# Kernel tuning notes

Measured on AMD Instinct MI355X. Metric: run time of the kernel, lower is better.

The kernel has to match this reference:

```python
import jax, jax.numpy as jnp
import numpy as np


def setup_inputs() -> dict:
    key = jax.random.key(0)
    d_model, state_dim, L = 512, 64, 2048
    scale = 1.0 / np.sqrt(state_dim)
    k1, k2, k3, k4, k5 = jax.random.split(key, 5)
    log_dt_min, log_dt_max = np.log(1e-3), np.log(0.1)
    return {
        "Lambda_re": jax.random.normal(k1, (d_model, state_dim), jnp.float32),
        "Lambda_im": jax.random.normal(k2, (d_model, state_dim), jnp.float32),
        "B_re": jax.random.normal(k3, (d_model, state_dim), jnp.float32) * scale,
        "B_im": jnp.zeros((d_model, state_dim), jnp.float32),
        "C_re": jax.random.normal(k4, (d_model, state_dim), jnp.float32) * scale,
        "C_im": jnp.zeros((d_model, state_dim), jnp.float32),
        "D": jnp.ones((d_model,), jnp.float32),
        "log_dt": jax.random.uniform(k5, (d_model,), jnp.float32, log_dt_min, log_dt_max),
        "L": L,
    }


def reference(Lambda_re, Lambda_im, B_re, B_im, C_re, C_im, D, log_dt, L):
    # Bilinear (Tustin) discretization of the diagonal SSM
    lam = (-jax.nn.softplus(Lambda_re) + 1j * Lambda_im).astype(jnp.complex64)  # (d, n)
    B = (B_re + 1j * B_im).astype(jnp.complex64)
    C = (C_re + 1j * C_im).astype(jnp.complex64)
    dt = jnp.exp(log_dt)[:, None]                 # (d, 1)
    half = 0.5 * dt * lam
    denom = 1.0 - half
    a_bar = (1.0 + half) / denom                  # (d, n)
    b_bar = dt / denom * B                        # (d, n)
    # Vandermonde power sum: K[d, l] = Re sum_n (C*b_bar)[d, n] * a_bar[d, n]**l
    k = jnp.arange(L, dtype=jnp.float32)
    a_pow = jnp.exp(jnp.log(a_bar)[:, :, None] * k)   # (d, n, L) complex
    K = jnp.einsum("dn,dnl->dl", C * b_bar, a_pow).real  # (d, L)
    return (K, D)
```

## Files before the change

kernel.cpp:

```cpp
#include <hip/hip_runtime.h>
#include <math.h>


#define STATE_DIM 64
#define BLOCK 256

__global__ __launch_bounds__(BLOCK) void lssl_kernel(
    const float* __restrict__ Lre, const float* __restrict__ Lim,
    const float* __restrict__ Bre, const float* __restrict__ Bim,
    const float* __restrict__ Cre, const float* __restrict__ Cim,
    const float* __restrict__ Dv,  const float* __restrict__ log_dt,
    float* __restrict__ out, int d_model, int L)
{
    const int d   = blockIdx.x;
    const int tid = threadIdx.x;

    __shared__ float s_log2r[STATE_DIM];
    __shared__ float s_threv[STATE_DIM];
    __shared__ float s_wre[STATE_DIM];
    __shared__ float s_wim[STATE_DIM];

    if (tid < STATE_DIM) {
        const int n   = tid;
        const int idx = d * STATE_DIM + n;
        float x      = Lre[idx];
        float sp     = fmaxf(x, 0.0f) + log1pf(expf(-fabsf(x)));
        float lam_re = -sp;
        float lam_im = Lim[idx];
        float dt     = expf(log_dt[d]);
        float hre    = 0.5f * dt * lam_re;
        float him    = 0.5f * dt * lam_im;
        float dre = 1.0f - hre, dim = -him;
        float inv = 1.0f / (dre * dre + dim * dim);
        float nre = 1.0f + hre, nim = him;
        float are = (nre * dre + nim * dim) * inv;
        float aim = (nim * dre - nre * dim) * inv;
        float idre = dre * inv, idim = -dim * inv;
        float bre = Bre[idx], bim = Bim[idx];
        float bbre = dt * (idre * bre - idim * bim);
        float bbim = dt * (idre * bim + idim * bre);
        float cre = Cre[idx], cim = Cim[idx];
        float wre = cre * bbre - cim * bbim;
        float wim = cre * bbim + cim * bbre;

        float r2 = are * are + aim * aim;
        s_log2r[n] = 0.5f * log2f(r2);
        s_threv[n] = atan2f(aim, are) * 0.15915494309189535f;
        s_wre[n]   = wre;
        s_wim[n]   = wim;
    }
    __syncthreads();

    const int l = blockIdx.y * BLOCK + tid;
    if (l < L) {
        const float fl = (float)l;
        float acc = 0.0f;
        #pragma unroll
        for (int n = 0; n < STATE_DIM; ++n) {
            float e = __builtin_amdgcn_exp2f(fl * s_log2r[n]);
            float t = fl * s_threv[n];
            t = t - floorf(t);
            float s = __builtin_amdgcn_sinf(t);
            float c = __builtin_amdgcn_cosf(t);
            acc += e * (s_wre[n] * c - s_wim[n] * s);
        }
        out[(size_t)d * L + l] = acc;
    }
    if (blockIdx.y == 0 && tid == 0) {
        out[(size_t)d_model * L + d] = Dv[d];
    }
}

extern "C" void kernel_launch(void* const* d_in, const int* in_sizes, int n_in,
                              void* d_out, int out_size, void* d_ws, size_t ws_size,
                              hipStream_t stream) {
    const float* Lre    = (const float*)d_in[0];
    const float* Lim    = (const float*)d_in[1];
    const float* Bre    = (const float*)d_in[2];
    const float* Bim    = (const float*)d_in[3];
    const float* Cre    = (const float*)d_in[4];
    const float* Cim    = (const float*)d_in[5];
    const float* Dv     = (const float*)d_in[6];
    const float* log_dt = (const float*)d_in[7];
    float* out = (float*)d_out;

    const int d_model = in_sizes[6];
    const int L       = out_size / d_model - 1;

    dim3 grid(d_model, (L + BLOCK - 1) / BLOCK);
    lssl_kernel<<<grid, BLOCK, 0, stream>>>(Lre, Lim, Bre, Bim, Cre, Cim, Dv, log_dt,
                                            out, d_model, L);
}
```

Before: 96.28 us.

## Replace per-position transcendentals with complex recurrence over strided positions

Each thread now handles LT=8 output positions spaced BLOCK apart. It computes exp2/sin/cos once per state for the first position, then reaches the others by repeated complex multiplication with a precomputed a^BLOCK, and parameters are packed into float4/float2 shared arrays. This removes most transcendental evaluations, which dominated the inner loop, in exchange for FMAs, possible accumulated rounding error, and a grid that shrinks to one block per d_model row (512 blocks).

```diff
diff --git a/kernel.cpp b/kernel.cpp
--- a/kernel.cpp
+++ b/kernel.cpp
@@ -4,6 +4,7 @@
 
 #define STATE_DIM 64
 #define BLOCK 256
+#define LT 8
 
 __global__ __launch_bounds__(BLOCK) void lssl_kernel(
     const float* __restrict__ Lre, const float* __restrict__ Lim,
@@ -15,10 +16,8 @@
     const int d   = blockIdx.x;
     const int tid = threadIdx.x;
 
-    __shared__ float s_log2r[STATE_DIM];
-    __shared__ float s_threv[STATE_DIM];
-    __shared__ float s_wre[STATE_DIM];
-    __shared__ float s_wim[STATE_DIM];
+    __shared__ float4 s_wa[STATE_DIM];
+    __shared__ float2 s_lt[STATE_DIM];
 
     if (tid < STATE_DIM) {
         const int n   = tid;
@@ -43,30 +42,59 @@
         float wre = cre * bbre - cim * bbim;
         float wim = cre * bbim + cim * bbre;
 
-        float r2 = are * are + aim * aim;
-        s_log2r[n] = 0.5f * log2f(r2);
-        s_threv[n] = atan2f(aim, are) * 0.15915494309189535f;
-        s_wre[n]   = wre;
-        s_wim[n]   = wim;
+        float r2    = are * are + aim * aim;
+        float log2r = 0.5f * log2f(r2);
+        float threv = atan2f(aim, are) * 0.15915494309189535f;
+
+        float eS = __builtin_amdgcn_exp2f((float)BLOCK * log2r);
+        float tS = (float)BLOCK * threv;
+        tS -= floorf(tS);
+        float aSre = eS * __builtin_amdgcn_cosf(tS);
+        float aSim = eS * __builtin_amdgcn_sinf(tS);
+
+        s_wa[n] = make_float4(wre, wim, aSre, aSim);
+        s_lt[n] = make_float2(log2r, threv);
     }
     __syncthreads();
 
-    const int l = blockIdx.y * BLOCK + tid;
-    if (l < L) {
-        const float fl = (float)l;
-        float acc = 0.0f;
+    const int l0 = blockIdx.y * (BLOCK * LT);
+    const float fl0 = (float)(l0 + tid);
+
+    float acc[LT];
+    #pragma unroll
+    for (int j = 0; j < LT; ++j) acc[j] = 0.0f;
+
+    #pragma unroll 4
+    for (int n = 0; n < STATE_DIM; ++n) {
+        float4 wa = s_wa[n];
+        float2 lt = s_lt[n];
+        float e = __builtin_amdgcn_exp2f(fl0 * lt.x);
+        float t = fl0 * lt.y;
+        t -= floorf(t);
+        float s = __builtin_amdgcn_sinf(t);
+        float c = __builtin_amdgcn_cosf(t);
+        float ure = e * c, uim = e * s;
+        float pre = wa.x * ure - wa.y * uim;
+        float pim = wa.x * uim + wa.y * ure;
+        acc[0] += pre;
         #pragma unroll
-        for (int n = 0; n < STATE_DIM; ++n) {
-            float e = __builtin_amdgcn_exp2f(fl * s_log2r[n]);
-            float t = fl * s_threv[n];
-            t = t - floorf(t);
-            float s = __builtin_amdgcn_sinf(t);
-            float c = __builtin_amdgcn_cosf(t);
-            acc += e * (s_wre[n] * c - s_wim[n] * s);
+        for (int j = 1; j < LT; ++j) {
+            float t0  = pre * wa.z;
+            float t1  = pre * wa.w;
+            float nr  = fmaf(-pim, wa.w, t0);
+            float ni  = fmaf( pim, wa.z, t1);
+            pre = nr; pim = ni;
+            acc[j] += pre;
         }
-        out[(size_t)d * L + l] = acc;
     }
-    if (blockIdx.y == 0 && tid == 0) {
+
+    float* orow = out + (size_t)d * L;
+    #pragma unroll
+    for (int j = 0; j < LT; ++j) {
+        int l = l0 + tid + j * BLOCK;
+        if (l < L) orow[l] = acc[j];
+    }
+    if (tid == 0 && blockIdx.y == 0) {
         out[(size_t)d_model * L + d] = Dv[d];
     }
 }
@@ -87,7 +115,8 @@
     const int d_model = in_sizes[6];
     const int L       = out_size / d_model - 1;
 
-    dim3 grid(d_model, (L + BLOCK - 1) / BLOCK);
+    const int chunk = BLOCK * LT;
+    dim3 grid(d_model, (L + chunk - 1) / chunk);
     lssl_kernel<<<grid, BLOCK, 0, stream>>>(Lre, Lim, Bre, Bim, Cre, Cim, Dv, log_dt,
                                             out, d_model, L);
 }
```

Measured after the change: 82.99 us. -13.8%, faster.
